# Kernel optimization log

Measured on AMD Instinct MI355X. Metric: run time of the kernel, lower is better.

Reference implementation:

```python
import jax, jax.numpy as jnp
import numpy as np

EPS = 1e-7

def _sample_project(feat, pid, w1, b1, w2, b2):
    # feat: [B, C, H, W]; pid: [P] flat spatial indices into H*W
    B, C, H, W = feat.shape
    fr = jnp.transpose(feat, (0, 2, 3, 1)).reshape(B, H * W, C)  # [B, HW, C]
    x = fr[:, pid, :].reshape(B * pid.shape[0], C)               # gather -> [B*P, C]
    x = jnp.maximum(x @ w1 + b1, 0.0) @ w2 + b2                  # 2-layer MLP
    norm = jnp.sqrt(jnp.sum(x * x, axis=1, keepdims=True))       # L2 over channels
    return x / (norm + EPS)


def setup_inputs() -> dict:
    key = jax.random.key(0)
    ks = jax.random.split(key, 16)
    NC = 256
    shapes = [(16, 256, 128, 128), (16, 512, 64, 64), (16, 1024, 32, 32)]
    inp = {}
    for i, s in enumerate(shapes):
        inp[f"feat{i}"] = jax.random.normal(ks[i], s, dtype=jnp.float32)
        hw = s[2] * s[3]
        inp[f"patch_id{i}"] = jax.random.randint(ks[3 + i], (256,), 0, hw, dtype=jnp.int64)
        C = s[1]
        g = 0.02  # init_gain (normal init)
        inp[f"w1_{i}"] = g * jax.random.normal(ks[6 + 3 * i], (C, NC), dtype=jnp.float32)
        inp[f"b1_{i}"] = jnp.zeros((NC,), dtype=jnp.float32)
        inp[f"w2_{i}"] = g * jax.random.normal(ks[7 + 3 * i], (NC, NC), dtype=jnp.float32)
        inp[f"b2_{i}"] = jnp.zeros((NC,), dtype=jnp.float32)
    return inp


def reference(feat0, feat1, feat2, patch_id0, patch_id1, patch_id2,
              w1_0, b1_0, w2_0, b2_0,
              w1_1, b1_1, w2_1, b2_1,
              w1_2, b1_2, w2_2, b2_2):
    out0 = _sample_project(feat0, patch_id0, w1_0, b1_0, w2_0, b2_0)
    out1 = _sample_project(feat1, patch_id1, w1_1, b1_1, w2_1, b2_1)
    out2 = _sample_project(feat2, patch_id2, w1_2, b1_2, w2_2, b2_2)
    return (out0, out1, out2)
```

## Files before the change

### kernel.cpp

```cpp
#include <hip/hip_runtime.h>

typedef __attribute__((ext_vector_type(8))) short short8;
typedef __attribute__((ext_vector_type(4))) float floatx4;
typedef __attribute__((ext_vector_type(4))) unsigned int uintx4;

__device__ __forceinline__ short f2bf(float f) {
    unsigned u = __builtin_bit_cast(unsigned, f);
    u = (u + 0x7FFFu + ((u >> 16) & 1u)) >> 16;
    return (short)u;
}


__global__ __launch_bounds__(256) void prep_w(
    const float* __restrict__ w10, const float* __restrict__ w11, const float* __restrict__ w12,
    const float* __restrict__ w20, const float* __restrict__ w21, const float* __restrict__ w22,
    unsigned short* __restrict__ wsb)
{
    __shared__ float tile[32][33];
    int blk = blockIdx.x;
    const float* in; unsigned short* out; int K, t0;
    if (blk < 64)       { in = w10; out = wsb;          K = 256;  t0 = 0; }
    else if (blk < 192) { in = w11; out = wsb + 65536;  K = 512;  t0 = 64; }
    else if (blk < 448) { in = w12; out = wsb + 196608; K = 1024; t0 = 192; }
    else if (blk < 512) { in = w20; out = wsb + 458752; K = 256;  t0 = 448; }
    else if (blk < 576) { in = w21; out = wsb + 524288; K = 256;  t0 = 512; }
    else                { in = w22; out = wsb + 589824; K = 256;  t0 = 576; }
    int tile_id = blk - t0;
    int tk = K >> 5;
    int k0 = (tile_id % tk) << 5;
    int n0 = (tile_id / tk) << 5;
    int t = threadIdx.x;
    int j = t & 31, i0 = (t >> 5) << 2;
    #pragma unroll
    for (int u = 0; u < 4; u++)
        tile[i0 + u][j] = in[(size_t)(k0 + i0 + u) * 256 + (n0 + j)];
    __syncthreads();
    int kf = t & 31, nf0 = (t >> 5) << 2;
    #pragma unroll
    for (int u = 0; u < 4; u++)
        out[(size_t)(n0 + nf0 + u) * K + (k0 + kf)] = (unsigned short)f2bf(tile[kf][nf0 + u]);
}

__global__ __launch_bounds__(256) void gather_x(
    const float* __restrict__ f0, const float* __restrict__ f1, const float* __restrict__ f2,
    const int* __restrict__ p0, const int* __restrict__ p1, const int* __restrict__ p2,
    unsigned short* __restrict__ xg)
{
    int blk = blockIdx.x;
    const float* feat; const int* pid; int C, HW, sh; unsigned short* dst;
    if (blk < 512)        { feat = f0; pid = p0; C = 256;  HW = 16384; sh = 5; dst = xg; }
    else if (blk < 1536)  { feat = f1; pid = p1; C = 512;  HW = 4096;  sh = 6; dst = xg + 1048576; blk -= 512; }
    else                  { feat = f2; pid = p2; C = 1024; HW = 1024;  sh = 7; dst = xg + 3145728; blk -= 1536; }

    int q   = (blk << 8) + threadIdx.x;
    int row = q >> sh;
    int c0  = (q & ((1 << sh) - 1)) << 3;
    int b   = row >> 8, pp = row & 255;
    int s   = pid[pp];
    const float* src = feat + ((size_t)b * C + c0) * HW + s;

    float v[8];
    #pragma unroll
    for (int j = 0; j < 8; j++) v[j] = src[(size_t)j * HW];
    short8 sv;
    #pragma unroll
    for (int j = 0; j < 8; j++) sv[j] = f2bf(v[j]);
    *(short8*)(dst + (size_t)row * C + c0) = sv;
}

__global__ __launch_bounds__(256) void mlp(
    const float* __restrict__ b1_0, const float* __restrict__ b1_1, const float* __restrict__ b1_2,
    const float* __restrict__ b2_0, const float* __restrict__ b2_1, const float* __restrict__ b2_2,
    const unsigned short* __restrict__ wsb,
    float* __restrict__ out)
{
    __shared__ __align__(16) unsigned short smem[26944];
    unsigned short* wsS = smem;
    unsigned short* hs  = smem + 18432;
    float* rs = (float*)(smem + 26880);

    int blk = blockIdx.x;
    int scale = 2 - (blk >> 7);
    int mblk = blk & 127;

    const float* b1; const float* b2;
    const unsigned short* w1T; const unsigned short* w2T; const unsigned short* xg;
    int C; size_t outBase;
    if (scale == 0)      { b1 = b1_0; b2 = b2_0; w1T = wsb;          w2T = wsb + 458752;
                           xg = wsb + 655360;           C = 256;  outBase = 0; }
    else if (scale == 1) { b1 = b1_1; b2 = b2_1; w1T = wsb + 65536;  w2T = wsb + 524288;
                           xg = wsb + 655360 + 1048576; C = 512;  outBase = 1048576; }
    else                 { b1 = b1_2; b2 = b2_2; w1T = wsb + 196608; w2T = wsb + 589824;
                           xg = wsb + 655360 + 3145728; C = 1024; outBase = 2097152; }

    int t = threadIdx.x;
    int wid = t >> 6, lane = t & 63, quad = lane >> 4, l15 = lane & 15;
    int r0 = (wid & 1) << 4;
    int c0 = (wid >> 1) << 7;

    floatx4 acc[8];
    #pragma unroll
    for (int f = 0; f < 8; f++) acc[f] = (floatx4){0.f, 0.f, 0.f, 0.f};

    const unsigned short* aG = xg + (size_t)((mblk << 5) + r0 + l15) * C;

    for (int kc = 0; kc < C; kc += 64) {
        {
            const uintx4* src = (const uintx4*)(w1T + (size_t)t * C + kc);
            uintx4* dst = (uintx4*)(wsS + t * 72);
            #pragma unroll
            for (int j2 = 0; j2 < 8; j2++) dst[j2] = src[j2];
        }
        __syncthreads();
        const unsigned short* bRow = wsS + (c0 + l15) * 72;
        #pragma unroll
        for (int ks = 0; ks < 2; ks++) {
            short8 af = *(const short8*)(aG + kc + ks * 32 + quad * 8);
            #pragma unroll
            for (int f = 0; f < 8; f++) {
                short8 bf = *(const short8*)(bRow + f * (16 * 72) + ks * 32 + quad * 8);
                acc[f] = __builtin_amdgcn_mfma_f32_16x16x32_bf16(af, bf, acc[f], 0, 0, 0);
            }
        }
        __syncthreads();
    }

    {
        float bias1[8];
        #pragma unroll
        for (int f = 0; f < 8; f++) bias1[f] = b1[c0 + f * 16 + l15];
        #pragma unroll
        for (int f = 0; f < 8; f++)
            #pragma unroll
            for (int reg = 0; reg < 4; reg++) {
                float h = fmaxf(acc[f][reg] + bias1[f], 0.f);
                hs[(r0 + quad * 4 + reg) * 264 + (c0 + f * 16 + l15)] = (unsigned short)f2bf(h);
            }
    }

    #pragma unroll
    for (int f = 0; f < 8; f++) acc[f] = (floatx4){0.f, 0.f, 0.f, 0.f};
    const unsigned short* hA = hs + (r0 + l15) * 264;
    for (int kc = 0; kc < 256; kc += 64) {
        {
            const uintx4* src = (const uintx4*)(w2T + (size_t)t * 256 + kc);
            uintx4* dst = (uintx4*)(wsS + t * 72);
            #pragma unroll
            for (int j2 = 0; j2 < 8; j2++) dst[j2] = src[j2];
        }
        __syncthreads();
        const unsigned short* bRow = wsS + (c0 + l15) * 72;
        #pragma unroll
        for (int ks = 0; ks < 2; ks++) {
            short8 af = *(const short8*)(hA + kc + ks * 32 + quad * 8);
            #pragma unroll
            for (int f = 0; f < 8; f++) {
                short8 bf = *(const short8*)(bRow + f * (16 * 72) + ks * 32 + quad * 8);
                acc[f] = __builtin_amdgcn_mfma_f32_16x16x32_bf16(af, bf, acc[f], 0, 0, 0);
            }
        }
        __syncthreads();
    }

    {
        float bias2[8];
        #pragma unroll
        for (int f = 0; f < 8; f++) bias2[f] = b2[c0 + f * 16 + l15];
        float psq[4] = {0.f, 0.f, 0.f, 0.f};
        #pragma unroll
        for (int f = 0; f < 8; f++)
            #pragma unroll
            for (int reg = 0; reg < 4; reg++) {
                float yv = acc[f][reg] + bias2[f];
                acc[f][reg] = yv;
                psq[reg] += yv * yv;
            }
        #pragma unroll
        for (int m = 1; m < 16; m <<= 1)
            #pragma unroll
            for (int reg = 0; reg < 4; reg++)
                psq[reg] += __shfl_xor(psq[reg], m, 16);

        if (t < 32) rs[t] = 0.f;
        __syncthreads();
        if (l15 == 0) {
            #pragma unroll
            for (int reg = 0; reg < 4; reg++)
                atomicAdd(&rs[r0 + quad * 4 + reg], psq[reg]);
        }
        __syncthreads();

        #pragma unroll
        for (int f = 0; f < 8; f++)
            #pragma unroll
            for (int reg = 0; reg < 4; reg++) {
                int row = r0 + quad * 4 + reg;
                float inv = 1.f / (sqrtf(rs[row]) + 1e-7f);
                out[outBase + (size_t)((mblk << 5) + row) * 256 + (c0 + f * 16 + l15)] =
                    acc[f][reg] * inv;
            }
    }
}

extern "C" void kernel_launch(void* const* d_in, const int* in_sizes, int n_in,
                              void* d_out, int out_size, void* d_ws, size_t ws_size,
                              hipStream_t stream)
{
    (void)n_in; (void)out_size; (void)ws_size;
    bool dict = (in_sizes[1] == 256);
    const float *feat[3], *w1[3], *b1[3], *w2[3], *b2[3];
    const int* pid[3];
    for (int i = 0; i < 3; i++) {
        if (dict) {
            feat[i] = (const float*)d_in[i * 6 + 0];
            pid[i]  = (const int*)  d_in[i * 6 + 1];
            w1[i]   = (const float*)d_in[i * 6 + 2];
            b1[i]   = (const float*)d_in[i * 6 + 3];
            w2[i]   = (const float*)d_in[i * 6 + 4];
            b2[i]   = (const float*)d_in[i * 6 + 5];
        } else {
            feat[i] = (const float*)d_in[i];
            pid[i]  = (const int*)  d_in[3 + i];
            w1[i]   = (const float*)d_in[6 + 4 * i + 0];
            b1[i]   = (const float*)d_in[6 + 4 * i + 1];
            w2[i]   = (const float*)d_in[6 + 4 * i + 2];
            b2[i]   = (const float*)d_in[6 + 4 * i + 3];
        }
    }
    unsigned short* wsb = (unsigned short*)d_ws;
    gather_x<<<3584, 256, 0, stream>>>(feat[0], feat[1], feat[2],
                                       pid[0], pid[1], pid[2],
                                       wsb + 655360);
    prep_w<<<640, 256, 0, stream>>>(w1[0], w1[1], w1[2], w2[0], w2[1], w2[2], wsb);
    mlp<<<384, 256, 0, stream>>>(b1[0], b1[1], b1[2],
                                 b2[0], b2[1], b2[2],
                                 wsb, (float*)d_out);
}
```

Measured before the change: 561.4 us.

## Stream scales 1-2 features coalesced via inverse-index LUT and shrink MLP tiles

For scales 1 and 2, the strided per-patch gather is replaced. A lookup table maps each spatial index to its patch slot, and blocks stream contiguous feature rows with vector loads, scattering the selected values through shared memory. This trades the uncoalesced strided reads for reading the full feature maps of those scales, which is more bytes overall. The MLP kernel now uses 16-row blocks with twice as many blocks and reads weights directly from global/L2 instead of staging them in LDS. Duplicate patch ids are resolved through the LUT, so rows are indexed by their last writer.

```diff
diff --git a/kernel.cpp b/kernel.cpp
--- a/kernel.cpp
+++ b/kernel.cpp
@@ -1,6 +1,7 @@
 #include <hip/hip_runtime.h>
 
 typedef __attribute__((ext_vector_type(8))) short short8;
+typedef __attribute__((ext_vector_type(4))) short short4v;
 typedef __attribute__((ext_vector_type(4))) float floatx4;
 typedef __attribute__((ext_vector_type(4))) unsigned int uintx4;
 
@@ -10,26 +11,50 @@
     return (short)u;
 }
 
-
-__global__ __launch_bounds__(256) void prep_w(
+#define W1T0 0
+#define W1T1 65536
+#define W1T2 196608
+#define W2T0 458752
+#define W2T1 524288
+#define W2T2 589824
+#define XG0  655360
+#define XG1  1703936
+#define XG2  3801088
+#define LUT0 7995392
+#define LUT1 8011776
+#define LUT2 8015872
+
+__global__ __launch_bounds__(256) void prep(
     const float* __restrict__ w10, const float* __restrict__ w11, const float* __restrict__ w12,
     const float* __restrict__ w20, const float* __restrict__ w21, const float* __restrict__ w22,
+    const int* __restrict__ p0, const int* __restrict__ p1, const int* __restrict__ p2,
     unsigned short* __restrict__ wsb)
 {
+    int blk = blockIdx.x;
+    int t = threadIdx.x;
+    if (blk == 640) {
+        short* lut = (short*)(wsb + LUT0);
+        for (int i = t; i < 21504; i += 256) lut[i] = -1;
+        __syncthreads();
+        if (t < 256) {
+            ((short*)(wsb + LUT0))[p0[t]] = (short)t;
+            ((short*)(wsb + LUT1))[p1[t]] = (short)t;
+            ((short*)(wsb + LUT2))[p2[t]] = (short)t;
+        }
+        return;
+    }
     __shared__ float tile[32][33];
-    int blk = blockIdx.x;
     const float* in; unsigned short* out; int K, t0;
-    if (blk < 64)       { in = w10; out = wsb;          K = 256;  t0 = 0; }
-    else if (blk < 192) { in = w11; out = wsb + 65536;  K = 512;  t0 = 64; }
-    else if (blk < 448) { in = w12; out = wsb + 196608; K = 1024; t0 = 192; }
-    else if (blk < 512) { in = w20; out = wsb + 458752; K = 256;  t0 = 448; }
-    else if (blk < 576) { in = w21; out = wsb + 524288; K = 256;  t0 = 512; }
-    else                { in = w22; out = wsb + 589824; K = 256;  t0 = 576; }
+    if (blk < 64)       { in = w10; out = wsb + W1T0; K = 256;  t0 = 0; }
+    else if (blk < 192) { in = w11; out = wsb + W1T1; K = 512;  t0 = 64; }
+    else if (blk < 448) { in = w12; out = wsb + W1T2; K = 1024; t0 = 192; }
+    else if (blk < 512) { in = w20; out = wsb + W2T0; K = 256;  t0 = 448; }
+    else if (blk < 576) { in = w21; out = wsb + W2T1; K = 256;  t0 = 512; }
+    else                { in = w22; out = wsb + W2T2; K = 256;  t0 = 576; }
     int tile_id = blk - t0;
     int tk = K >> 5;
     int k0 = (tile_id % tk) << 5;
     int n0 = (tile_id / tk) << 5;
-    int t = threadIdx.x;
     int j = t & 31, i0 = (t >> 5) << 2;
     #pragma unroll
     for (int u = 0; u < 4; u++)
@@ -41,165 +66,183 @@
         out[(size_t)(n0 + nf0 + u) * K + (k0 + kf)] = (unsigned short)f2bf(tile[kf][nf0 + u]);
 }
 
-__global__ __launch_bounds__(256) void gather_x(
+__global__ __launch_bounds__(256) void stage(
     const float* __restrict__ f0, const float* __restrict__ f1, const float* __restrict__ f2,
-    const int* __restrict__ p0, const int* __restrict__ p1, const int* __restrict__ p2,
-    unsigned short* __restrict__ xg)
-{
+    const int* __restrict__ p0,
+    unsigned short* __restrict__ wsb)
+{
+    __shared__ unsigned short tile[256 * 40];
+    __shared__ int flags[256];
     int blk = blockIdx.x;
-    const float* feat; const int* pid; int C, HW, sh; unsigned short* dst;
-    if (blk < 512)        { feat = f0; pid = p0; C = 256;  HW = 16384; sh = 5; dst = xg; }
-    else if (blk < 1536)  { feat = f1; pid = p1; C = 512;  HW = 4096;  sh = 6; dst = xg + 1048576; blk -= 512; }
-    else                  { feat = f2; pid = p2; C = 1024; HW = 1024;  sh = 7; dst = xg + 3145728; blk -= 1536; }
-
-    int q   = (blk << 8) + threadIdx.x;
-    int row = q >> sh;
-    int c0  = (q & ((1 << sh) - 1)) << 3;
-    int b   = row >> 8, pp = row & 255;
-    int s   = pid[pp];
-    const float* src = feat + ((size_t)b * C + c0) * HW + s;
-
-    float v[8];
-    #pragma unroll
-    for (int j = 0; j < 8; j++) v[j] = src[(size_t)j * HW];
-    short8 sv;
-    #pragma unroll
-    for (int j = 0; j < 8; j++) sv[j] = f2bf(v[j]);
-    *(short8*)(dst + (size_t)row * C + c0) = sv;
+    int t = threadIdx.x;
+
+    if (blk < 512) {
+        int q = (blk << 8) + t;
+        int row = q >> 5, c0 = (q & 31) << 3;
+        int b = row >> 8, pp = row & 255;
+        int s = p0[pp];
+        const float* src = f0 + ((size_t)b * 256 + c0) * 16384 + s;
+        float v[8];
+        #pragma unroll
+        for (int j = 0; j < 8; j++) v[j] = src[(size_t)j * 16384];
+        short8 sv;
+        #pragma unroll
+        for (int j = 0; j < 8; j++) sv[j] = f2bf(v[j]);
+        *(short8*)(wsb + XG0 + (size_t)row * 256 + c0) = sv;
+        return;
+    }
+
+    const float* feat; const short* lut; unsigned short* xg;
+    int C, HW, b, c0, hw0;
+    if (blk < 1536) {
+        int idx = blk - 512;
+        feat = f1; lut = (const short*)(wsb + LUT1); xg = wsb + XG1;
+        C = 512; HW = 4096;
+        b = idx >> 6; int rem = idx & 63;
+        c0 = (rem >> 2) << 5; hw0 = (rem & 3) << 10;
+    } else {
+        int idx = blk - 1536;
+        feat = f2; lut = (const short*)(wsb + LUT2); xg = wsb + XG2;
+        C = 1024; HW = 1024;
+        b = idx >> 5; c0 = (idx & 31) << 5; hw0 = 0;
+    }
+    flags[t] = 0;
+    __syncthreads();
+
+    int cl = t >> 3, sub = t & 7;
+    const float* fr = feat + ((size_t)b * C + c0 + cl) * HW + hw0;
+    const short* lr = lut + hw0;
+    for (int i = 0; i < 32; i++) {
+        int hw = i * 32 + sub * 4;
+        floatx4 v = *(const floatx4*)(fr + hw);
+        short4v l4 = *(const short4v*)(lr + hw);
+        #pragma unroll
+        for (int j = 0; j < 4; j++) {
+            int pv = l4[j];
+            if (pv >= 0) {
+                tile[pv * 40 + cl] = (unsigned short)f2bf(v[j]);
+                flags[pv] = 1;
+            }
+        }
+    }
+    __syncthreads();
+    if (flags[t]) {
+        uintx4* d = (uintx4*)(xg + (size_t)(b * 256 + t) * C + c0);
+        const uintx4* s4 = (const uintx4*)(tile + t * 40);
+        d[0] = s4[0]; d[1] = s4[1]; d[2] = s4[2]; d[3] = s4[3];
+    }
 }
 
 __global__ __launch_bounds__(256) void mlp(
     const float* __restrict__ b1_0, const float* __restrict__ b1_1, const float* __restrict__ b1_2,
     const float* __restrict__ b2_0, const float* __restrict__ b2_1, const float* __restrict__ b2_2,
+    const int* __restrict__ p0, const int* __restrict__ p1, const int* __restrict__ p2,
     const unsigned short* __restrict__ wsb,
     float* __restrict__ out)
 {
-    __shared__ __align__(16) unsigned short smem[26944];
-    unsigned short* wsS = smem;
-    unsigned short* hs  = smem + 18432;
-    float* rs = (float*)(smem + 26880);
+    __shared__ __align__(16) unsigned short hs[16 * 264];
+    __shared__ float rs[16];
 
     int blk = blockIdx.x;
-    int scale = 2 - (blk >> 7);
-    int mblk = blk & 127;
-
-    const float* b1; const float* b2;
-    const unsigned short* w1T; const unsigned short* w2T; const unsigned short* xg;
+    int scale = 2 - (blk >> 8);
+    int mblk = blk & 255;
+
+    const float *b1, *b2; const int* pid;
+    const unsigned short *w1T, *w2T, *xg; const short* lut;
     int C; size_t outBase;
-    if (scale == 0)      { b1 = b1_0; b2 = b2_0; w1T = wsb;          w2T = wsb + 458752;
-                           xg = wsb + 655360;           C = 256;  outBase = 0; }
-    else if (scale == 1) { b1 = b1_1; b2 = b2_1; w1T = wsb + 65536;  w2T = wsb + 524288;
-                           xg = wsb + 655360 + 1048576; C = 512;  outBase = 1048576; }
-    else                 { b1 = b1_2; b2 = b2_2; w1T = wsb + 196608; w2T = wsb + 589824;
-                           xg = wsb + 655360 + 3145728; C = 1024; outBase = 2097152; }
-
-    int t = threadIdx.x;
-    int wid = t >> 6, lane = t & 63, quad = lane >> 4, l15 = lane & 15;
-    int r0 = (wid & 1) << 4;
-    int c0 = (wid >> 1) << 7;
-
-    floatx4 acc[8];
-    #pragma unroll
-    for (int f = 0; f < 8; f++) acc[f] = (floatx4){0.f, 0.f, 0.f, 0.f};
-
-    const unsigned short* aG = xg + (size_t)((mblk << 5) + r0 + l15) * C;
+    if (scale == 0)      { b1 = b1_0; b2 = b2_0; pid = p0; lut = (const short*)(wsb + LUT0);
+                           w1T = wsb + W1T0; w2T = wsb + W2T0; xg = wsb + XG0; C = 256;  outBase = 0; }
+    else if (scale == 1) { b1 = b1_1; b2 = b2_1; pid = p1; lut = (const short*)(wsb + LUT1);
+                           w1T = wsb + W1T1; w2T = wsb + W2T1; xg = wsb + XG1; C = 512;  outBase = 1048576; }
+    else                 { b1 = b1_2; b2 = b2_2; pid = p2; lut = (const short*)(wsb + LUT2);
+                           w1T = wsb + W1T2; w2T = wsb + W2T2; xg = wsb + XG2; C = 1024; outBase = 2097152; }
+
+    int t = threadIdx.x, wid = t >> 6, lane = t & 63, quad = lane >> 4, l15 = lane & 15;
+    int c0 = wid << 6;
+    int rowBase = mblk << 4;
+    int myRow = rowBase + l15;
+    int b = myRow >> 8, pp = myRow & 255;
+    int w = lut[pid[pp]];
+    const unsigned short* aBase = xg + (size_t)(b * 256 + w) * C;
+
+    floatx4 acc[4];
+    #pragma unroll
+    for (int f = 0; f < 4; f++) acc[f] = (floatx4){0.f, 0.f, 0.f, 0.f};
 
     for (int kc = 0; kc < C; kc += 64) {
-        {
-            const uintx4* src = (const uintx4*)(w1T + (size_t)t * C + kc);
-            uintx4* dst = (uintx4*)(wsS + t * 72);
-            #pragma unroll
-            for (int j2 = 0; j2 < 8; j2++) dst[j2] = src[j2];
-        }
-        __syncthreads();
-        const unsigned short* bRow = wsS + (c0 + l15) * 72;
-        #pragma unroll
-        for (int ks = 0; ks < 2; ks++) {
-            short8 af = *(const short8*)(aG + kc + ks * 32 + quad * 8);
-            #pragma unroll
-            for (int f = 0; f < 8; f++) {
-                short8 bf = *(const short8*)(bRow + f * (16 * 72) + ks * 32 + quad * 8);
-                acc[f] = __builtin_amdgcn_mfma_f32_16x16x32_bf16(af, bf, acc[f], 0, 0, 0);
-            }
-        }
-        __syncthreads();
-    }
-
-    {
-        float bias1[8];
-        #pragma unroll
-        for (int f = 0; f < 8; f++) bias1[f] = b1[c0 + f * 16 + l15];
-        #pragma unroll
-        for (int f = 0; f < 8; f++)
-            #pragma unroll
-            for (int reg = 0; reg < 4; reg++) {
-                float h = fmaxf(acc[f][reg] + bias1[f], 0.f);
-                hs[(r0 + quad * 4 + reg) * 264 + (c0 + f * 16 + l15)] = (unsigned short)f2bf(h);
-            }
-    }
-
-    #pragma unroll
-    for (int f = 0; f < 8; f++) acc[f] = (floatx4){0.f, 0.f, 0.f, 0.f};
-    const unsigned short* hA = hs + (r0 + l15) * 264;
+        short8 a0 = *(const short8*)(aBase + kc + quad * 8);
+        short8 a1 = *(const short8*)(aBase + kc + 32 + quad * 8);
+        #pragma unroll
+        for (int f = 0; f < 4; f++) {
+            const unsigned short* wr = w1T + (size_t)(c0 + f * 16 + l15) * C + kc;
+            short8 bv0 = *(const short8*)(wr + quad * 8);
+            short8 bv1 = *(const short8*)(wr + 32 + quad * 8);
+            acc[f] = __builtin_amdgcn_mfma_f32_16x16x32_bf16(a0, bv0, acc[f], 0, 0, 0);
+            acc[f] = __builtin_amdgcn_mfma_f32_16x16x32_bf16(a1, bv1, acc[f], 0, 0, 0);
+        }
+    }
+
+    #pragma unroll
+    for (int f = 0; f < 4; f++) {
+        float bias = b1[c0 + f * 16 + l15];
+        #pragma unroll
+        for (int r = 0; r < 4; r++) {
+            float h = fmaxf(acc[f][r] + bias, 0.f);
+            hs[(quad * 4 + r) * 264 + (c0 + f * 16 + l15)] = (unsigned short)f2bf(h);
+        }
+    }
+    if (t < 16) rs[t] = 0.f;
+    __syncthreads();
+
+    #pragma unroll
+    for (int f = 0; f < 4; f++) acc[f] = (floatx4){0.f, 0.f, 0.f, 0.f};
+    const unsigned short* hA = hs + l15 * 264;
     for (int kc = 0; kc < 256; kc += 64) {
-        {
-            const uintx4* src = (const uintx4*)(w2T + (size_t)t * 256 + kc);
-            uintx4* dst = (uintx4*)(wsS + t * 72);
-            #pragma unroll
-            for (int j2 = 0; j2 < 8; j2++) dst[j2] = src[j2];
-        }
-        __syncthreads();
-        const unsigned short* bRow = wsS + (c0 + l15) * 72;
-        #pragma unroll
-        for (int ks = 0; ks < 2; ks++) {
-            short8 af = *(const short8*)(hA + kc + ks * 32 + quad * 8);
-            #pragma unroll
-            for (int f = 0; f < 8; f++) {
-                short8 bf = *(const short8*)(bRow + f * (16 * 72) + ks * 32 + quad * 8);
-                acc[f] = __builtin_amdgcn_mfma_f32_16x16x32_bf16(af, bf, acc[f], 0, 0, 0);
-            }
-        }
-        __syncthreads();
-    }
-
-    {
-        float bias2[8];
-        #pragma unroll
-        for (int f = 0; f < 8; f++) bias2[f] = b2[c0 + f * 16 + l15];
-        float psq[4] = {0.f, 0.f, 0.f, 0.f};
-        #pragma unroll
-        for (int f = 0; f < 8; f++)
-            #pragma unroll
-            for (int reg = 0; reg < 4; reg++) {
-                float yv = acc[f][reg] + bias2[f];
-                acc[f][reg] = yv;
-                psq[reg] += yv * yv;
-            }
-        #pragma unroll
-        for (int m = 1; m < 16; m <<= 1)
-            #pragma unroll
-            for (int reg = 0; reg < 4; reg++)
-                psq[reg] += __shfl_xor(psq[reg], m, 16);
-
-        if (t < 32) rs[t] = 0.f;
-        __syncthreads();
-        if (l15 == 0) {
-            #pragma unroll
-            for (int reg = 0; reg < 4; reg++)
-                atomicAdd(&rs[r0 + quad * 4 + reg], psq[reg]);
-        }
-        __syncthreads();
-
-        #pragma unroll
-        for (int f = 0; f < 8; f++)
-            #pragma unroll
-            for (int reg = 0; reg < 4; reg++) {
-                int row = r0 + quad * 4 + reg;
-                float inv = 1.f / (sqrtf(rs[row]) + 1e-7f);
-                out[outBase + (size_t)((mblk << 5) + row) * 256 + (c0 + f * 16 + l15)] =
-                    acc[f][reg] * inv;
-            }
-    }
+        short8 a0 = *(const short8*)(hA + kc + quad * 8);
+        short8 a1 = *(const short8*)(hA + kc + 32 + quad * 8);
+        #pragma unroll
+        for (int f = 0; f < 4; f++) {
+            const unsigned short* wr = w2T + (size_t)(c0 + f * 16 + l15) * 256 + kc;
+            short8 bv0 = *(const short8*)(wr + quad * 8);
+            short8 bv1 = *(const short8*)(wr + 32 + quad * 8);
+            acc[f] = __builtin_amdgcn_mfma_f32_16x16x32_bf16(a0, bv0, acc[f], 0, 0, 0);
+            acc[f] = __builtin_amdgcn_mfma_f32_16x16x32_bf16(a1, bv1, acc[f], 0, 0, 0);
+        }
+    }
+
+    float bias2[4];
+    #pragma unroll
+    for (int f = 0; f < 4; f++) bias2[f] = b2[c0 + f * 16 + l15];
+    float psq[4] = {0.f, 0.f, 0.f, 0.f};
+    #pragma unroll
+    for (int f = 0; f < 4; f++)
+        #pragma unroll
+        for (int r = 0; r < 4; r++) {
+            float yv = acc[f][r] + bias2[f];
+            acc[f][r] = yv;
+            psq[r] += yv * yv;
+        }
+    #pragma unroll
+    for (int m = 1; m < 16; m <<= 1)
+        #pragma unroll
+        for (int r = 0; r < 4; r++)
+            psq[r] += __shfl_xor(psq[r], m, 16);
+    if (l15 == 0) {
+        #pragma unroll
+        for (int r = 0; r < 4; r++)
+            atomicAdd(&rs[quad * 4 + r], psq[r]);
+    }
+    __syncthreads();
+
+    #pragma unroll
+    for (int f = 0; f < 4; f++)
+        #pragma unroll
+        for (int r = 0; r < 4; r++) {
+            int row = quad * 4 + r;
+            float inv = 1.f / (sqrtf(rs[row]) + 1e-7f);
+            out[outBase + (size_t)(rowBase + row) * 256 + (c0 + f * 16 + l15)] =
+                acc[f][r] * inv;
+        }
 }
 
 extern "C" void kernel_launch(void* const* d_in, const int* in_sizes, int n_in,
@@ -228,11 +271,11 @@
         }
     }
     unsigned short* wsb = (unsigned short*)d_ws;
-    gather_x<<<3584, 256, 0, stream>>>(feat[0], feat[1], feat[2],
-                                       pid[0], pid[1], pid[2],
-                                       wsb + 655360);
-    prep_w<<<640, 256, 0, stream>>>(w1[0], w1[1], w1[2], w2[0], w2[1], w2[2], wsb);
-    mlp<<<384, 256, 0, stream>>>(b1[0], b1[1], b1[2],
+    prep<<<641, 256, 0, stream>>>(w1[0], w1[1], w1[2], w2[0], w2[1], w2[2],
+                                  pid[0], pid[1], pid[2], wsb);
+    stage<<<2048, 256, 0, stream>>>(feat[0], feat[1], feat[2], pid[0], wsb);
+    mlp<<<768, 256, 0, stream>>>(b1[0], b1[1], b1[2],
                                  b2[0], b2[1], b2[2],
+                                 pid[0], pid[1], pid[2],
                                  wsb, (float*)d_out);
 }
```

After: 548.4 us. 1.02x faster.
